# Kernel optimization log

Measured on AMD Instinct MI355X. Metric: run time of the kernel, lower is better.

Reference implementation:

```python
import jax, jax.numpy as jnp
import numpy as np

N_NODES = 50000
N_EDGES = 800000
D_FEAT = 128
UNITS = 256
K = 3


def setup_inputs() -> dict:
    key = jax.random.key(0)
    k1, k2, k3, k4 = jax.random.split(key, 4)
    x = jax.random.normal(k1, (N_NODES, D_FEAT), dtype=jnp.float32)
    edge_index = jax.random.randint(k2, (2, N_EDGES), 0, N_NODES, dtype=jnp.int32)
    edge_weight = jnp.ones((N_EDGES,), dtype=jnp.float32)
    # glorot-uniform kernel [(K+1)*D, UNITS], zero bias
    fan_in, fan_out = D_FEAT * (K + 1), UNITS
    limit = np.sqrt(6.0 / (fan_in + fan_out)).astype(np.float32)
    kernel = jax.random.uniform(k3, (fan_in, fan_out), minval=-limit, maxval=limit, dtype=jnp.float32)
    bias = jnp.zeros((UNITS,), dtype=jnp.float32)
    return {"x": x, "edge_index": edge_index, "edge_weight": edge_weight,
            "kernel": kernel, "bias": bias}


def reference(x, edge_index, edge_weight, kernel, bias):
    n = x.shape[0]
    row, col = edge_index[0], edge_index[1]
    # symmetric GCN normalization (renorm=False: normalize first, then self-loops w=1)
    deg = jax.ops.segment_sum(edge_weight, row, num_segments=n)
    deg_inv_sqrt = jnp.where(deg > 0, jax.lax.rsqrt(jnp.where(deg > 0, deg, 1.0)), 0.0)
    normed_w = deg_inv_sqrt[row] * edge_weight * deg_inv_sqrt[col]
    loop = jnp.arange(n, dtype=row.dtype)
    row2 = jnp.concatenate([row, loop])
    col2 = jnp.concatenate([col, loop])
    w2 = jnp.concatenate([normed_w, jnp.ones((n,), dtype=normed_w.dtype)])
    # K-hop propagation, collecting each hop
    xs = [x]
    h = x
    for _ in range(K):
        msg = h[col2] * w2[:, None]            # [E+N, D] gather + scale
        h = jax.ops.segment_sum(msg, row2, num_segments=n)  # scatter-sum
        xs.append(h)
    hcat = jnp.concatenate(xs, axis=-1)        # [N, (K+1)*D]
    out = hcat @ kernel + bias
    return jax.nn.relu(out)
```

## Files before the change

kernel.cpp:

```cpp
#include <hip/hip_runtime.h>

#define NN 50000
#define NP 50048
#define NE 800000
#define D 128
#define UNITS 256
#define KTOT 512
#define SCAN_NB 50
#define NREP 16
#define CONV_NB 6250

typedef __attribute__((ext_vector_type(8))) short short8;
typedef __attribute__((ext_vector_type(4))) float floatx4;

__device__ inline unsigned short f2b(float f) {
    unsigned u = __float_as_uint(f);
    return (unsigned short)((u + 0x7fff + ((u >> 16) & 1)) >> 16);
}
__device__ inline float2 bx2f(unsigned v) {
    float2 r;
    r.x = __uint_as_float(v << 16);
    r.y = __uint_as_float(v & 0xffff0000u);
    return r;
}

__global__ void count_kernel(const int* __restrict__ row, int* __restrict__ cnt16,
                             int* __restrict__ rank, int E) {
    int e = blockIdx.x * blockDim.x + threadIdx.x;
    if (e < E) {
        int rep = (e >> 6) & (NREP - 1);
        rank[e] = atomicAdd(&cnt16[rep * NN + row[e]], 1);
    }
}

__global__ __launch_bounds__(256) void scanA_kernel(int* __restrict__ cnt16,
                                                    int* __restrict__ row_ptr,
                                                    int* __restrict__ bsum) {
    __shared__ int s[256];
    int b = blockIdx.x, t = threadIdx.x;
    int base = b * 1024 + t * 4;
    int v[4];
    int sum = 0;
#pragma unroll
    for (int i = 0; i < 4; ++i) {
        int idx = base + i;
        int tot = 0;
        if (idx < NN) {
            int c[NREP];
            int run = 0;
#pragma unroll
            for (int r = 0; r < NREP; ++r) c[r] = cnt16[r * NN + idx];
#pragma unroll
            for (int r = 0; r < NREP; ++r) {
                cnt16[r * NN + idx] = run;
                run += c[r];
            }
            tot = run;
        }
        v[i] = tot;
        sum += tot;
    }
    s[t] = sum;
    __syncthreads();
    for (int off = 1; off < 256; off <<= 1) {
        int add = (t >= off) ? s[t - off] : 0;
        __syncthreads();
        s[t] += add;
        __syncthreads();
    }
    int run = s[t] - sum;
#pragma unroll
    for (int i = 0; i < 4; ++i) {
        int idx = base + i;
        if (idx < NN) row_ptr[idx] = run;
        run += v[i];
    }
    if (t == 255) bsum[b] = s[255];
}

__global__ void scanB_kernel(int* __restrict__ bsum, int* __restrict__ row_ptr) {
    if (threadIdx.x == 0 && blockIdx.x == 0) {
        int run = 0;
        for (int i = 0; i < SCAN_NB; ++i) {
            int v = bsum[i];
            bsum[i] = run;
            run += v;
        }
        row_ptr[NN] = run;
    }
}

__global__ __launch_bounds__(256) void scanC_kernel(int* __restrict__ row_ptr,
                                                    const int* __restrict__ bsum) {
    int b = blockIdx.x, t = threadIdx.x;
    int off = bsum[b];
    int base = b * 1024 + t * 4;
#pragma unroll
    for (int i = 0; i < 4; ++i) {
        int idx = base + i;
        if (idx < NN) row_ptr[idx] += off;
    }
}

__global__ void fill_kernel(const int* __restrict__ row, const int* __restrict__ col,
                            const float* __restrict__ w, const int* __restrict__ rank,
                            const int* __restrict__ row_ptr, const int* __restrict__ cnt16,
                            int2* __restrict__ edges, int E) {
    int e = blockIdx.x * blockDim.x + threadIdx.x;
    if (e >= E) return;
    int r = row[e];
    int rep = (e >> 6) & (NREP - 1);
    int pos = row_ptr[r] + cnt16[rep * NN + r] + rank[e];
    edges[pos] = make_int2(col[e], __float_as_int(w[e]));
}

__global__ __launch_bounds__(256) void degdis_kernel(const int* __restrict__ row_ptr,
                                                     const int2* __restrict__ edges,
                                                     float* __restrict__ dis) {
    int node = blockIdx.x * 4 + (threadIdx.x >> 6);
    int l = threadIdx.x & 63;
    if (node >= NN) return;
    int beg = row_ptr[node], end = row_ptr[node + 1];
    float s = 0.f;
    for (int e = beg + l; e < end; e += 64) s += __int_as_float(edges[e].y);
#pragma unroll
    for (int off = 32; off; off >>= 1) s += __shfl_down(s, off);
    if (l == 0) dis[node] = s > 0.f ? rsqrtf(s) : 0.f;
}

__global__ __launch_bounds__(256) void prep_kernel(const float* __restrict__ x,
                                                   unsigned* __restrict__ xb,
                                                   const float* __restrict__ W,
                                                   short* __restrict__ Wt) {
    __shared__ float tile[32][33];
    if (blockIdx.x < CONV_NB) {
        int t = blockIdx.x * 256 + threadIdx.x;
        float4 v = ((const float4*)x)[t];
        uint2 o;
        o.x = (unsigned)f2b(v.x) | ((unsigned)f2b(v.y) << 16);
        o.y = (unsigned)f2b(v.z) | ((unsigned)f2b(v.w) << 16);
        ((uint2*)xb)[t] = o;
    } else {
        int b = blockIdx.x - CONV_NB;
        int kb = (b & 15) * 32;
        int nb = (b >> 4) * 32;
        int tx = threadIdx.x & 31, ty = threadIdx.x >> 5;
        for (int i = 0; i < 32; i += 8)
            tile[ty + i][tx] = W[(size_t)(kb + ty + i) * UNITS + nb + tx];
        __syncthreads();
        for (int i = 0; i < 32; i += 8)
            Wt[(size_t)(nb + ty + i) * KTOT + kb + tx] = (short)f2b(tile[tx][ty + i]);
    }
}

__device__ inline void acc8(float* acc, uint4 v, float w) {
    float2 f0 = bx2f(v.x), f1 = bx2f(v.y), f2 = bx2f(v.z), f3 = bx2f(v.w);
    acc[0] = fmaf(w, f0.x, acc[0]); acc[1] = fmaf(w, f0.y, acc[1]);
    acc[2] = fmaf(w, f1.x, acc[2]); acc[3] = fmaf(w, f1.y, acc[3]);
    acc[4] = fmaf(w, f2.x, acc[4]); acc[5] = fmaf(w, f2.y, acc[5]);
    acc[6] = fmaf(w, f3.x, acc[6]); acc[7] = fmaf(w, f3.y, acc[7]);
}

template <bool NORM>
__global__ __launch_bounds__(256) void gather_kernel(const unsigned* __restrict__ hprev,
                                                     unsigned* __restrict__ hnext,
                                                     const int* __restrict__ row_ptr,
                                                     int2* __restrict__ edges,
                                                     const float* __restrict__ dis) {
    int node = blockIdx.x * 4 + (threadIdx.x >> 6);
    if (node >= NN) return;
    int l = threadIdx.x & 63;
    int g = l >> 4;
    int s = l & 15;
    const uint4* hp4 = (const uint4*)hprev;
    int beg = row_ptr[node], end = row_ptr[node + 1];
    float dr = NORM ? dis[node] : 1.f;

    float acc[8] = {0.f, 0.f, 0.f, 0.f, 0.f, 0.f, 0.f, 0.f};
    int2 M0 = edges[(beg + g) < end ? (beg + g) : end - 1];
    int2 M1 = edges[(beg + 4 + g) < end ? (beg + 4 + g) : end - 1];
    for (int e = beg; e < end; e += 8) {
        int i0 = e + g;
        int i1 = e + 4 + g;
        int2 E0 = M0, E1 = M1;
        int en = e + 8;
        if (en < end) {
            int j0 = en + g, j1 = en + 4 + g;
            M0 = edges[j0 < end ? j0 : end - 1];
            M1 = edges[j1 < end ? j1 : end - 1];
        }
        float w0 = __int_as_float(E0.y);
        float w1 = __int_as_float(E1.y);
        if (NORM) {
            w0 *= dr * dis[E0.x];
            w1 *= dr * dis[E1.x];
        }
        w0 = (i0 < end) ? w0 : 0.f;
        w1 = (i1 < end) ? w1 : 0.f;
        uint4 v0 = hp4[(size_t)E0.x * 16 + s];
        uint4 v1 = hp4[(size_t)E1.x * 16 + s];
        acc8(acc, v0, w0);
        acc8(acc, v1, w1);
        if (NORM && s == 0) {
            if (i0 < end) edges[i0].y = __float_as_int(w0);
            if (i1 < end) edges[i1].y = __float_as_int(w1);
        }
    }
#pragma unroll
    for (int i = 0; i < 8; ++i) {
        acc[i] += __shfl_xor(acc[i], 16);
        acc[i] += __shfl_xor(acc[i], 32);
    }
    if (g == 0) {
        uint4 sv = hp4[(size_t)node * 16 + s];
        acc8(acc, sv, 1.f);
        uint4 o;
        o.x = (unsigned)f2b(acc[0]) | ((unsigned)f2b(acc[1]) << 16);
        o.y = (unsigned)f2b(acc[2]) | ((unsigned)f2b(acc[3]) << 16);
        o.z = (unsigned)f2b(acc[4]) | ((unsigned)f2b(acc[5]) << 16);
        o.w = (unsigned)f2b(acc[6]) | ((unsigned)f2b(acc[7]) << 16);
        ((uint4*)hnext)[(size_t)node * 16 + s] = o;
    }
}

#define BK 64
#define GLDS(g, l)                                                                      \
    __builtin_amdgcn_global_load_lds((const __attribute__((address_space(1))) void*)(g), \
                                     (__attribute__((address_space(3))) void*)(l), 16, 0, 0)

__global__ __launch_bounds__(256) void gemm_mfma(const short* __restrict__ A0,
                                                 const short* __restrict__ Wt,
                                                 const float* __restrict__ bias,
                                                 float* __restrict__ C) {
    __shared__ short As[128 * BK];
    __shared__ short Bs[128 * BK];
    const int t = threadIdx.x;
    const int m0 = blockIdx.x * 128;
    const int n0 = blockIdx.y * 128;
    const int w = t >> 6;
    const int l = t & 63;
    const int wr = (w >> 1) * 64;
    const int wc = (w & 1) * 64;
    const int lm = l & 15;
    const int lg = l >> 4;

    const int srow = l >> 3;
    const int soff = ((l & 7) ^ srow) * 8;

    floatx4 zero = {0.f, 0.f, 0.f, 0.f};
    floatx4 acc[4][4];
#pragma unroll
    for (int r = 0; r < 4; ++r)
#pragma unroll
        for (int c = 0; c < 4; ++c) acc[r][c] = zero;

    for (int kk = 0; kk < KTOT; kk += BK) {
        const short* Asrc = A0 + (size_t)(kk >> 7) * ((size_t)NP * 128) + (kk & 127);
        const short* Bsrc = Wt + kk;
#pragma unroll
        for (int i = 0; i < 4; ++i) {
            int seg = w * 4 + i;
            int row = seg * 8 + srow;
            GLDS(Asrc + (size_t)(m0 + row) * D + soff, As + seg * 512);
            GLDS(Bsrc + (size_t)(n0 + row) * KTOT + soff, Bs + seg * 512);
        }
        __syncthreads();
#pragma unroll
        for (int j = 0; j < 2; ++j) {
            short8 af[4], bfr[4];
#pragma unroll
            for (int r = 0; r < 4; ++r) {
                int row = wr + r * 16 + lm;
                int ch = (lg + 4 * j) ^ (row & 7);
                af[r] = *(const short8*)&As[row * BK + ch * 8];
            }
#pragma unroll
            for (int c = 0; c < 4; ++c) {
                int row = wc + c * 16 + lm;
                int ch = (lg + 4 * j) ^ (row & 7);
                bfr[c] = *(const short8*)&Bs[row * BK + ch * 8];
            }
#pragma unroll
            for (int r = 0; r < 4; ++r)
#pragma unroll
                for (int c = 0; c < 4; ++c)
                    acc[r][c] = __builtin_amdgcn_mfma_f32_16x16x32_bf16(af[r], bfr[c],
                                                                        acc[r][c], 0, 0, 0);
        }
        __syncthreads();
    }

    const int q4 = lg * 4;
#pragma unroll
    for (int r = 0; r < 4; ++r) {
#pragma unroll
        for (int i = 0; i < 4; ++i) {
            int m = m0 + wr + r * 16 + q4 + i;
            if (m < NN) {
#pragma unroll
                for (int c = 0; c < 4; ++c) {
                    int n = n0 + wc + c * 16 + lm;
                    float v = acc[r][c][i] + bias[n];
                    C[(size_t)m * UNITS + n] = fmaxf(v, 0.f);
                }
            }
        }
    }
}

extern "C" void kernel_launch(void* const* d_in, const int* in_sizes, int n_in,
                              void* d_out, int out_size, void* d_ws, size_t ws_size,
                              hipStream_t stream) {
    const float* x = (const float*)d_in[0];
    const int* ei = (const int*)d_in[1];
    const float* ew_in = (const float*)d_in[2];
    const float* W = (const float*)d_in[3];
    const float* bias = (const float*)d_in[4];
    float* out = (float*)d_out;

    const int* row = ei;
    const int* col = ei + NE;

    float* dis = (float*)d_ws;
    int* cnt16 = (int*)(dis + NN);
    int* rank = cnt16 + NREP * NN;
    int* bsum = rank + NE;
    int* row_ptr = bsum + 64;
    int2* edges = (int2*)(row_ptr + NN + 2);
    unsigned* xb = (unsigned*)(edges + NE) + 2;
    unsigned* h1b = xb + (size_t)NP * 64;
    unsigned* h2b = h1b + (size_t)NP * 64;
    unsigned* h3b = h2b + (size_t)NP * 64;
    short* Wt = (short*)(h3b + (size_t)NP * 64);

    hipMemsetAsync(cnt16, 0, NREP * NN * sizeof(int), stream);

    count_kernel<<<(NE + 255) / 256, 256, 0, stream>>>(row, cnt16, rank, NE);
    scanA_kernel<<<SCAN_NB, 256, 0, stream>>>(cnt16, row_ptr, bsum);
    scanB_kernel<<<1, 64, 0, stream>>>(bsum, row_ptr);
    scanC_kernel<<<SCAN_NB, 256, 0, stream>>>(row_ptr, bsum);
    fill_kernel<<<(NE + 255) / 256, 256, 0, stream>>>(row, col, ew_in, rank, row_ptr, cnt16,
                                                      edges, NE);
    degdis_kernel<<<(NN + 3) / 4, 256, 0, stream>>>(row_ptr, edges, dis);
    prep_kernel<<<CONV_NB + 128, 256, 0, stream>>>(x, xb, W, Wt);

    int gat_blocks = (NN + 3) / 4;
    gather_kernel<true><<<gat_blocks, 256, 0, stream>>>(xb, h1b, row_ptr, edges, dis);
    gather_kernel<false><<<gat_blocks, 256, 0, stream>>>(h1b, h2b, row_ptr, edges, dis);
    gather_kernel<false><<<gat_blocks, 256, 0, stream>>>(h2b, h3b, row_ptr, edges, dis);

    gemm_mfma<<<dim3(NP / 128, UNITS / 128), 256, 0, stream>>>(
        (const short*)xb, Wt, bias, out);
}
```

Baseline: 315.4 us.

## Replace LDS-staged GEMM with direct global-to-register MFMA loads

The final GEMM no longer stages A and B tiles through shared memory with barriers. Each wave now loads its MFMA fragments straight from global memory. A block covers 64 rows and all 256 output columns, one 64-column slice per wave, which gives a 1D grid over rows. This removes LDS traffic and __syncthreads but relies on L1/L2 for reuse of the shared A rows across the four waves, and issues less coalesced 16-byte loads.

```diff
diff --git a/kernel.cpp b/kernel.cpp
--- a/kernel.cpp
+++ b/kernel.cpp
@@ -223,29 +223,17 @@
     }
 }
 
-#define BK 64
-#define GLDS(g, l)                                                                      \
-    __builtin_amdgcn_global_load_lds((const __attribute__((address_space(1))) void*)(g), \
-                                     (__attribute__((address_space(3))) void*)(l), 16, 0, 0)
-
 __global__ __launch_bounds__(256) void gemm_mfma(const short* __restrict__ A0,
                                                  const short* __restrict__ Wt,
                                                  const float* __restrict__ bias,
                                                  float* __restrict__ C) {
-    __shared__ short As[128 * BK];
-    __shared__ short Bs[128 * BK];
     const int t = threadIdx.x;
-    const int m0 = blockIdx.x * 128;
-    const int n0 = blockIdx.y * 128;
-    const int w = t >> 6;
+    const int wn = t >> 6;
     const int l = t & 63;
-    const int wr = (w >> 1) * 64;
-    const int wc = (w & 1) * 64;
     const int lm = l & 15;
     const int lg = l >> 4;
-
-    const int srow = l >> 3;
-    const int soff = ((l & 7) ^ srow) * 8;
+    const int m0 = blockIdx.x * 64;
+    const int n0 = wn * 64;
 
     floatx4 zero = {0.f, 0.f, 0.f, 0.f};
     floatx4 acc[4][4];
@@ -254,52 +242,35 @@
 #pragma unroll
         for (int c = 0; c < 4; ++c) acc[r][c] = zero;
 
-    for (int kk = 0; kk < KTOT; kk += BK) {
-        const short* Asrc = A0 + (size_t)(kk >> 7) * ((size_t)NP * 128) + (kk & 127);
-        const short* Bsrc = Wt + kk;
+#pragma unroll 4
+    for (int ks = 0; ks < KTOT; ks += 32) {
+        const short* Asrc = A0 + (size_t)(ks >> 7) * ((size_t)NP * D) + (ks & 127) + lg * 8;
+        const short* Bsrc = Wt + ks + lg * 8;
+        short8 af[4], bfr[4];
+#pragma unroll
+        for (int r = 0; r < 4; ++r)
+            af[r] = *(const short8*)(Asrc + (size_t)(m0 + r * 16 + lm) * D);
+#pragma unroll
+        for (int c = 0; c < 4; ++c)
+            bfr[c] = *(const short8*)(Bsrc + (size_t)(n0 + c * 16 + lm) * KTOT);
+#pragma unroll
+        for (int r = 0; r < 4; ++r)
+#pragma unroll
+            for (int c = 0; c < 4; ++c)
+                acc[r][c] = __builtin_amdgcn_mfma_f32_16x16x32_bf16(af[r], bfr[c],
+                                                                    acc[r][c], 0, 0, 0);
+    }
+
+    const int q4 = lg * 4;
+#pragma unroll
+    for (int r = 0; r < 4; ++r) {
 #pragma unroll
         for (int i = 0; i < 4; ++i) {
-            int seg = w * 4 + i;
-            int row = seg * 8 + srow;
-            GLDS(Asrc + (size_t)(m0 + row) * D + soff, As + seg * 512);
-            GLDS(Bsrc + (size_t)(n0 + row) * KTOT + soff, Bs + seg * 512);
-        }
-        __syncthreads();
-#pragma unroll
-        for (int j = 0; j < 2; ++j) {
-            short8 af[4], bfr[4];
-#pragma unroll
-            for (int r = 0; r < 4; ++r) {
-                int row = wr + r * 16 + lm;
-                int ch = (lg + 4 * j) ^ (row & 7);
-                af[r] = *(const short8*)&As[row * BK + ch * 8];
-            }
-#pragma unroll
-            for (int c = 0; c < 4; ++c) {
-                int row = wc + c * 16 + lm;
-                int ch = (lg + 4 * j) ^ (row & 7);
-                bfr[c] = *(const short8*)&Bs[row * BK + ch * 8];
-            }
-#pragma unroll
-            for (int r = 0; r < 4; ++r)
-#pragma unroll
-                for (int c = 0; c < 4; ++c)
-                    acc[r][c] = __builtin_amdgcn_mfma_f32_16x16x32_bf16(af[r], bfr[c],
-                                                                        acc[r][c], 0, 0, 0);
-        }
-        __syncthreads();
-    }
-
-    const int q4 = lg * 4;
-#pragma unroll
-    for (int r = 0; r < 4; ++r) {
-#pragma unroll
-        for (int i = 0; i < 4; ++i) {
-            int m = m0 + wr + r * 16 + q4 + i;
+            int m = m0 + r * 16 + q4 + i;
             if (m < NN) {
 #pragma unroll
                 for (int c = 0; c < 4; ++c) {
-                    int n = n0 + wc + c * 16 + lm;
+                    int n = n0 + c * 16 + lm;
                     float v = acc[r][c][i] + bias[n];
                     C[(size_t)m * UNITS + n] = fmaxf(v, 0.f);
                 }
@@ -349,6 +320,5 @@
     gather_kernel<false><<<gat_blocks, 256, 0, stream>>>(h1b, h2b, row_ptr, edges, dis);
     gather_kernel<false><<<gat_blocks, 256, 0, stream>>>(h2b, h3b, row_ptr, edges, dis);
 
-    gemm_mfma<<<dim3(NP / 128, UNITS / 128), 256, 0, stream>>>(
-        (const short*)xb, Wt, bias, out);
-}
+    gemm_mfma<<<NP / 64, 256, 0, stream>>>((const short*)xb, Wt, bias, out);
+}
```

After: 342.3 us. +8.5%, slower.
